# Kernel tuning notes

Hardware: AMD Instinct MI355X
Metric: run time of the kernel (lower is better)

## Reference

```python
import jax, jax.numpy as jnp
import numpy as np

N_NODES = 50000
IN_C = 128
OUT_C = 128
N_EDGES = 1600000
NEG_SLOPE = 0.2
EPS = 1e-16  # matches torch_geometric softmax denominator epsilon


def setup_inputs() -> dict:
    key = jax.random.key(0)
    k1, k2, k3, k4, k5 = jax.random.split(key, 5)
    glorot = 1.0 / np.sqrt(IN_C)
    x = jax.random.normal(k1, (N_NODES, IN_C), dtype=jnp.float32)
    W = jax.random.normal(k2, (IN_C, OUT_C), dtype=jnp.float32) * glorot
    a_src = jax.random.normal(k3, (OUT_C,), dtype=jnp.float32) * glorot
    a_dst = jax.random.normal(k4, (OUT_C,), dtype=jnp.float32) * glorot
    bias = jnp.zeros((OUT_C,), dtype=jnp.float32)
    edge_index = jax.random.randint(k5, (2, N_EDGES), 0, N_NODES, dtype=jnp.int32)
    return {"x": x, "W": W, "a_src": a_src, "a_dst": a_dst,
            "bias": bias, "edge_index": edge_index}


def reference(x, W, a_src, a_dst, bias, edge_index):
    N = x.shape[0]
    # add self loops (GATConv default add_self_loops=True)
    loops = jnp.arange(N, dtype=edge_index.dtype)
    src = jnp.concatenate([edge_index[0], loops])  # [E+N]
    dst = jnp.concatenate([edge_index[1], loops])

    h = x @ W                                      # [N, out]
    alpha_s = h @ a_src                            # [N]
    alpha_d = h @ a_dst                            # [N]

    e = alpha_s[src] + alpha_d[dst]                # [E+N]
    e = jnp.where(e > 0, e, NEG_SLOPE * e)         # leaky_relu

    # neighbor-wise (per destination node) stable softmax
    m = jax.ops.segment_max(e, dst, num_segments=N)
    ex = jnp.exp(e - m[dst])
    denom = jax.ops.segment_sum(ex, dst, num_segments=N)
    alpha = ex / (denom[dst] + EPS)

    # weighted aggregation of source features into destination nodes
    msgs = h[src] * alpha[:, None]                 # [E+N, out]
    out = jax.ops.segment_sum(msgs, dst, num_segments=N) + bias
    return jax.nn.relu(out)
```

## Files before the change

kernel.cpp:

```cpp
#include <hip/hip_runtime.h>
#include <hip/hip_fp16.h>

#define C 128
#define NEG_SLOPE 0.2f
#define SM_EPS 1e-16f
#define BKT_SHIFT 8
#define BKT_MASK 255
#define WP 136

typedef unsigned int uint32;
typedef __attribute__((ext_vector_type(8))) short bf16x8;
typedef __attribute__((ext_vector_type(4))) float f32x4;

static __device__ __forceinline__ unsigned short f2bf(float f) {
    uint32 u = __float_as_uint(f);
    uint32 r = 0x7FFFu + ((u >> 16) & 1u);
    return (unsigned short)((u + r) >> 16);
}
static __device__ __forceinline__ uint32 f2bf2(float lo, float hi) {
    return (uint32)f2bf(lo) | ((uint32)f2bf(hi) << 16);
}
static __device__ __forceinline__ uint32 f2h(float f) {
    __half h = __float2half(f);
    return (uint32)*reinterpret_cast<unsigned short*>(&h);
}
static __device__ __forceinline__ float h2f(uint32 b) {
    unsigned short s = (unsigned short)(b & 0xffffu);
    __half h = *reinterpret_cast<__half*>(&s);
    return __half2float(h);
}

__global__ __launch_bounds__(256) void cvtw_kernel(const float* __restrict__ W,
                                                   uint32* __restrict__ Wf) {
    int gid = blockIdx.x * 256 + threadIdx.x;
    int j2   = gid & 3;
    int lane = (gid >> 2) & 63;
    int tile = gid >> 8;
    int t = tile >> 2, kk = tile & 3;
    int n = t * 16 + (lane & 15);
    int k = kk * 32 + (lane >> 4) * 8 + j2 * 2;
    Wf[gid] = f2bf2(W[k * C + n], W[(k + 1) * C + n]);
}

__global__ __launch_bounds__(256) void gemm_hist_kernel(
    const float* __restrict__ x, const uint32* __restrict__ Wf,
    const float* __restrict__ a_src, const float* __restrict__ a_dst,
    unsigned short* __restrict__ hb, float* __restrict__ as_out,
    float* __restrict__ ad_out, int N,
    const int* __restrict__ dst, int* __restrict__ H,
    int E, int total, int chunkE)
{
    __shared__ __align__(16) unsigned short slice[4][16 * WP];
    __shared__ int lhist[256];

    const int tid  = threadIdx.x;
    const int lane = tid & 63;
    const int w    = tid >> 6;
    const int row0 = blockIdx.x * 64;
    const int m16  = lane & 15;
    const int q    = lane >> 4;

    lhist[tid] = 0;

    const int row = row0 + w * 16 + m16;
    const bool rv = (row < N);
    const float* xr_p = x + (size_t)(rv ? row : 0) * C + q * 8;

    float4 xr[8];
    #pragma unroll
    for (int kk = 0; kk < 4; ++kk) {
        xr[kk * 2]     = rv ? *(const float4*)(xr_p + kk * 32)     : make_float4(0, 0, 0, 0);
        xr[kk * 2 + 1] = rv ? *(const float4*)(xr_p + kk * 32 + 4) : make_float4(0, 0, 0, 0);
    }

    f32x4 acc[8];
    const f32x4 zz = {0.f, 0.f, 0.f, 0.f};
    #pragma unroll
    for (int t = 0; t < 8; ++t) acc[t] = zz;

    #pragma unroll
    for (int kk = 0; kk < 4; ++kk) {
        union { bf16x8 v; uint32 u[4]; } au;
        float4 p0 = xr[kk * 2], p1 = xr[kk * 2 + 1];
        au.u[0] = f2bf2(p0.x, p0.y); au.u[1] = f2bf2(p0.z, p0.w);
        au.u[2] = f2bf2(p1.x, p1.y); au.u[3] = f2bf2(p1.z, p1.w);
        #pragma unroll
        for (int t = 0; t < 8; ++t) {
            bf16x8 b = *(const bf16x8*)&Wf[((t * 4 + kk) * 64 + lane) * 4];
            acc[t] = __builtin_amdgcn_mfma_f32_16x16x32_bf16(au.v, b, acc[t], 0, 0, 0);
        }
    }

    float ps[4] = {0.f, 0.f, 0.f, 0.f}, pd[4] = {0.f, 0.f, 0.f, 0.f};
    #pragma unroll
    for (int t = 0; t < 8; ++t) {
        float av = a_src[t * 16 + m16];
        float dv = a_dst[t * 16 + m16];
        #pragma unroll
        for (int r = 0; r < 4; ++r) {
            ps[r] += acc[t][r] * av;
            pd[r] += acc[t][r] * dv;
        }
    }
    #pragma unroll
    for (int r = 0; r < 4; ++r) {
        #pragma unroll
        for (int off = 1; off < 16; off <<= 1) {
            ps[r] += __shfl_xor(ps[r], off, 64);
            pd[r] += __shfl_xor(pd[r], off, 64);
        }
    }
    if (m16 == 0) {
        #pragma unroll
        for (int r = 0; r < 4; ++r) {
            int rr = row0 + w * 16 + q * 4 + r;
            if (rr < N) { as_out[rr] = ps[r]; ad_out[rr] = pd[r]; }
        }
    }

    #pragma unroll
    for (int t = 0; t < 8; ++t)
        #pragma unroll
        for (int r = 0; r < 4; ++r)
            slice[w][(q * 4 + r) * WP + t * 16 + m16] = f2bf(acc[t][r]);
    __syncthreads();
    #pragma unroll
    for (int it = 0; it < 4; ++it) {
        int r = it * 4 + q;
        int rr = row0 + w * 16 + r;
        if (rr < N) {
            bf16x8 v = *(const bf16x8*)&slice[w][r * WP + m16 * 8];
            *(bf16x8*)&hb[(size_t)rr * C + m16 * 8] = v;
        }
    }

    const int c = blockIdx.x;
    const int start = c * chunkE;
    const int end = min(start + chunkE, total);
    for (int i = start + tid; i < end; i += 256) {
        int d = (i < E) ? dst[i] : (i - E);
        atomicAdd(&lhist[d >> BKT_SHIFT], 1);
    }
    __syncthreads();
    H[c * 256 + tid] = lhist[tid];
}

__global__ __launch_bounds__(1024) void scan_cols_kernel(
    int* __restrict__ H, int* __restrict__ colTot, int nchunk)
{
    __shared__ int wt[16];
    const int tid  = threadIdx.x;
    const int lane = tid & 63;
    const int w    = tid >> 6;
    const int col  = blockIdx.x;
    int v = (tid < nchunk) ? H[tid * 256 + col] : 0;
    int x = v;
    #pragma unroll
    for (int o = 1; o < 64; o <<= 1) {
        int t = __shfl_up(x, o, 64);
        if (lane >= o) x += t;
    }
    if (lane == 63) wt[w] = x;
    __syncthreads();
    int wbase = 0;
    #pragma unroll
    for (int w2 = 0; w2 < 16; ++w2) wbase += (w2 < w) ? wt[w2] : 0;
    int e = wbase + x - v;
    if (tid < nchunk) H[tid * 256 + col] = e;
    if (tid == nchunk - 1) colTot[col] = e + v;
}

__global__ __launch_bounds__(256) void scan_off_kernel(
    const int* __restrict__ colTot, int* __restrict__ bucket_off, int total)
{
    __shared__ int wt[4];
    const int tid = threadIdx.x;
    const int lane = tid & 63;
    const int w = tid >> 6;
    int v = colTot[tid];
    int x = v;
    #pragma unroll
    for (int o = 1; o < 64; o <<= 1) {
        int t = __shfl_up(x, o, 64);
        if (lane >= o) x += t;
    }
    if (lane == 63) wt[w] = x;
    __syncthreads();
    int wbase = 0;
    #pragma unroll
    for (int w2 = 0; w2 < 4; ++w2) wbase += (w2 < w) ? wt[w2] : 0;
    bucket_off[tid] = wbase + x - v;
    if (tid == 0) bucket_off[256] = total;
}

__global__ __launch_bounds__(256) void bin_kernel(
    const int* __restrict__ src, const int* __restrict__ dst,
    const int* __restrict__ bucket_off, const int* __restrict__ H,
    uint32* __restrict__ packed, int E, int total, int chunkE)
{
    __shared__ int lhist[256];
    __shared__ int base[256];
    const int tid = threadIdx.x;
    const int c = blockIdx.x;
    const int start = c * chunkE;
    const int end = min(start + chunkE, total);

    lhist[tid] = 0;
    __syncthreads();
    for (int i = start + tid; i < end; i += 256) {
        int d = (i < E) ? dst[i] : (i - E);
        atomicAdd(&lhist[d >> BKT_SHIFT], 1);
    }
    __syncthreads();
    base[tid] = bucket_off[tid] + H[c * 256 + tid];
    lhist[tid] = 0;
    __syncthreads();
    for (int i = start + tid; i < end; i += 256) {
        int s = (i < E) ? src[i] : (i - E);
        int d = (i < E) ? dst[i] : (i - E);
        int b = d >> BKT_SHIFT;
        int pos = base[b] + atomicAdd(&lhist[b], 1);
        packed[pos] = ((uint32)s << BKT_SHIFT) | (uint32)(d & BKT_MASK);
    }
}

__global__ __launch_bounds__(1024) void build_kernel(
    const uint32* __restrict__ packed, const int* __restrict__ bucket_off,
    const float* __restrict__ as, const float* __restrict__ ad,
    int* __restrict__ row_start, uint32* __restrict__ csr, int N, int NB, int total)
{
    __shared__ int cnt[256];
    __shared__ int cur[256];
    __shared__ float adl[256];
    __shared__ int wt[4];
    const int tid = threadIdx.x;
    const int b = blockIdx.x;

    if (tid < 256) {
        cnt[tid] = 0;
        int g = (b << BKT_SHIFT) + tid;
        adl[tid] = (g < N) ? ad[g] : 0.f;
    }
    __syncthreads();
    const int off = bucket_off[b];
    const int end = bucket_off[b + 1];
    if (b == 0 && tid == 0) row_start[N] = total;

    for (int j = off + tid; j < end; j += 1024)
        atomicAdd(&cnt[packed[j] & BKT_MASK], 1);
    __syncthreads();

    int v2 = 0, x2 = 0;
    if (tid < 256) {
        const int lane = tid & 63;
        v2 = cnt[tid]; x2 = v2;
        #pragma unroll
        for (int o = 1; o < 64; o <<= 1) {
            int t = __shfl_up(x2, o, 64);
            if (lane >= o) x2 += t;
        }
        if (lane == 63) wt[tid >> 6] = x2;
    }
    __syncthreads();
    if (tid < 256) {
        const int w = tid >> 6;
        int wbase = 0;
        #pragma unroll
        for (int w2 = 0; w2 < 4; ++w2) wbase += (w2 < w) ? wt[w2] : 0;
        int excl = wbase + x2 - v2;
        int g = (b << BKT_SHIFT) + tid;
        if (g < N) row_start[g] = off + excl;
        cur[tid] = excl;
    }
    __syncthreads();

    for (int j = off + tid; j < end; j += 1024) {
        uint32 p = packed[j];
        int l = (int)(p & BKT_MASK);
        int s = (int)(p >> BKT_SHIFT);
        float e = as[s] + adl[l];
        e = (e > 0.f) ? e : NEG_SLOPE * e;
        int pos = atomicAdd(&cur[l], 1);
        csr[off + pos] = ((uint32)s << 16) | f2h(e);
    }
}

static __device__ __forceinline__ void gather_node_fw(
    int d, const uint32* __restrict__ csr, const int* __restrict__ row_start,
    const unsigned short* __restrict__ hb, const float* __restrict__ bias,
    float* __restrict__ out, int lane)
{
    const int beg = row_start[d];
    const int deg = row_start[d + 1] - beg;
    const int c2 = lane << 1;
    float a0 = 0.f, a1 = 0.f;
    float m = -INFINITY;
    for (int t = lane; t < deg; t += 64) m = fmaxf(m, h2f(csr[beg + t]));
    #pragma unroll
    for (int off = 32; off > 0; off >>= 1) m = fmaxf(m, __shfl_xor(m, off, 64));
    float ssum = 0.f;
    for (int t = lane; t < deg; t += 64) ssum += __expf(h2f(csr[beg + t]) - m);
    #pragma unroll
    for (int off = 32; off > 0; off >>= 1) ssum += __shfl_xor(ssum, off, 64);
    float inv = 1.f / (ssum + SM_EPS);
    for (int t0 = 0; t0 < deg; t0 += 64) {
        int nc = min(64, deg - t0);
        uint32 ent = (lane < nc) ? csr[beg + t0 + lane] : 0xFC00u;
        float wl = (lane < nc) ? __expf(h2f(ent) - m) * inv : 0.f;
        uint32 bc = (ent & 0xffff0000u) | f2h(wl);
        for (int t = 0; t < nc; ++t) {
            uint32 b0 = (uint32)__shfl((int)bc, t, 64);
            uint32 u0 = *(const uint32*)&hb[(size_t)(b0 >> 16) * C + c2];
            float w0 = h2f(b0);
            a0 += __uint_as_float(u0 << 16) * w0;
            a1 += __uint_as_float(u0 & 0xffff0000u) * w0;
        }
    }
    float2 b2 = *(const float2*)&bias[c2];
    a0 = fmaxf(a0 + b2.x, 0.f);
    a1 = fmaxf(a1 + b2.y, 0.f);
    *(float2*)&out[(size_t)d * C + c2] = make_float2(a0, a1);
}

#define ACC4(r, wgt)                                           \
    {                                                          \
        a0 += __uint_as_float((r).x << 16)         * (wgt);    \
        a1 += __uint_as_float((r).x & 0xffff0000u) * (wgt);    \
        a2 += __uint_as_float((r).y << 16)         * (wgt);    \
        a3 += __uint_as_float((r).y & 0xffff0000u) * (wgt);    \
    }

__global__ __launch_bounds__(256) void gather_kernel(
    const uint32* __restrict__ csr, const int* __restrict__ row_start,
    const unsigned short* __restrict__ hb, const float* __restrict__ bias,
    float* __restrict__ out, int N)
{
    __shared__ __align__(16) uint2 lent[4][2][64];
    const int w    = threadIdx.x >> 6;
    const int lane = threadIdx.x & 63;
    const int half = lane >> 5;
    const int hl   = lane & 31;
    const int pair = blockIdx.x * 4 + w;
    const int d0 = pair * 2;
    if (d0 >= N) return;
    const int d = d0 + half;
    const bool valid = (d < N);

    int beg = 0, deg = 0;
    if (valid) { beg = row_start[d]; deg = row_start[d + 1] - beg; }

    int wdeg = deg;
    #pragma unroll
    for (int off = 32; off > 0; off >>= 1) wdeg = max(wdeg, __shfl_xor(wdeg, off, 64));

    if (wdeg > 64) {
        gather_node_fw(d0, csr, row_start, hb, bias, out, lane);
        if (d0 + 1 < N) gather_node_fw(d0 + 1, csr, row_start, hb, bias, out, lane);
        return;
    }

    uint32 ent0 = (hl < deg) ? csr[beg + hl] : 0xFC00u;
    uint32 ent1 = (32 + hl < deg) ? csr[beg + 32 + hl] : 0xFC00u;
    float e0 = h2f(ent0), e1 = h2f(ent1);
    float m = fmaxf(e0, e1);
    #pragma unroll
    for (int off = 16; off > 0; off >>= 1) m = fmaxf(m, __shfl_xor(m, off, 64));
    float p0 = (hl < deg) ? __expf(e0 - m) : 0.f;
    float p1 = (32 + hl < deg) ? __expf(e1 - m) : 0.f;
    float ssum = p0 + p1;
    #pragma unroll
    for (int off = 16; off > 0; off >>= 1) ssum += __shfl_xor(ssum, off, 64);
    const float inv = 1.f / (ssum + SM_EPS);

    lent[w][half][hl]      = make_uint2((ent0 & 0xffff0000u) >> 8, __float_as_uint(p0 * inv));
    lent[w][half][32 + hl] = make_uint2((ent1 & 0xffff0000u) >> 8, __float_as_uint(p1 * inv));
    __builtin_amdgcn_wave_barrier();

    const uint32 cb = (uint32)(hl << 3);
    const char* hbB = (const char*)hb;
    const uint2* lp = &lent[w][half][0];
    float a0 = 0.f, a1 = 0.f, a2 = 0.f, a3 = 0.f;

    int t = 0;
    for (; t + 8 <= deg; t += 8) {
        uint4 q0 = *(const uint4*)(lp + t);
        uint4 q1 = *(const uint4*)(lp + t + 2);
        uint4 q2 = *(const uint4*)(lp + t + 4);
        uint4 q3 = *(const uint4*)(lp + t + 6);
        uint2 r0 = *(const uint2*)(hbB + (q0.x + cb));
        uint2 r1 = *(const uint2*)(hbB + (q0.z + cb));
        uint2 r2 = *(const uint2*)(hbB + (q1.x + cb));
        uint2 r3 = *(const uint2*)(hbB + (q1.z + cb));
        uint2 r4 = *(const uint2*)(hbB + (q2.x + cb));
        uint2 r5 = *(const uint2*)(hbB + (q2.z + cb));
        uint2 r6 = *(const uint2*)(hbB + (q3.x + cb));
        uint2 r7 = *(const uint2*)(hbB + (q3.z + cb));
        float w0 = __uint_as_float(q0.y), w1 = __uint_as_float(q0.w);
        float w2 = __uint_as_float(q1.y), w3 = __uint_as_float(q1.w);
        float w4 = __uint_as_float(q2.y), w5 = __uint_as_float(q2.w);
        float w6 = __uint_as_float(q3.y), w7 = __uint_as_float(q3.w);
        ACC4(r0, w0) ACC4(r1, w1) ACC4(r2, w2) ACC4(r3, w3)
        ACC4(r4, w4) ACC4(r5, w5) ACC4(r6, w6) ACC4(r7, w7)
    }
    for (; t < deg; ++t) {
        uint2 q = lp[t];
        uint2 r = *(const uint2*)(hbB + (q.x + cb));
        float wt = __uint_as_float(q.y);
        ACC4(r, wt)
    }

    if (valid) {
        const int c4 = hl << 2;
        float4 bb = *(const float4*)&bias[c4];
        float4 o;
        o.x = fmaxf(a0 + bb.x, 0.f);
        o.y = fmaxf(a1 + bb.y, 0.f);
        o.z = fmaxf(a2 + bb.z, 0.f);
        o.w = fmaxf(a3 + bb.w, 0.f);
        *(float4*)&out[(size_t)d * C + c4] = o;
    }
}

extern "C" void kernel_launch(void* const* d_in, const int* in_sizes, int n_in,
                              void* d_out, int out_size, void* d_ws, size_t ws_size,
                              hipStream_t stream) {
    const float* x     = (const float*)d_in[0];
    const float* W     = (const float*)d_in[1];
    const float* a_src = (const float*)d_in[2];
    const float* a_dst = (const float*)d_in[3];
    const float* bias  = (const float*)d_in[4];
    const int*   edge  = (const int*)d_in[5];

    const int N = in_sizes[0] / C;
    const int E = in_sizes[5] / 2;
    const int total = E + N;
    const int* src = edge;
    const int* dst = edge + E;
    float* out = (float*)d_out;

    const int NB = (N + BKT_MASK) >> BKT_SHIFT;
    const int ntile = (N + 63) / 64;
    const int chunkE = (total + ntile - 1) / ntile;

    float* ws = (float*)d_ws;
    unsigned short* hb = (unsigned short*)ws;
    float* as = (float*)(hb + (size_t)N * C);
    float* ad = as + N;
    int* row_start = (int*)(ad + N);
    uint32* packed = (uint32*)(row_start + (N + 2));
    uint32* csr    = packed + total;
    uint32* Wf     = csr + total;
    int* colTot    = (int*)(Wf + 8192);
    int* bucket_off = colTot + 256;
    int* H          = bucket_off + 257;

    cvtw_kernel<<<32, 256, 0, stream>>>(W, Wf);
    gemm_hist_kernel<<<ntile, 256, 0, stream>>>(
        x, Wf, a_src, a_dst, hb, as, ad, N, dst, H, E, total, chunkE);
    scan_cols_kernel<<<256, 1024, 0, stream>>>(H, colTot, ntile);
    scan_off_kernel<<<1, 256, 0, stream>>>(colTot, bucket_off, total);
    bin_kernel<<<ntile, 256, 0, stream>>>(
        src, dst, bucket_off, H, packed, E, total, chunkE);
    build_kernel<<<NB, 1024, 0, stream>>>(packed, bucket_off, as, ad, row_start,
                                          csr, N, NB, total);
    gather_kernel<<<((N + 1) / 2 + 3) / 4, 256, 0, stream>>>(csr, row_start, hb, bias, out, N);
}
```

Baseline: 187.6 us.

## Split GEMM across bin/build kernels and compute attention logits via precomposed W·a

Attention scalars are now computed as x·(W·a) in fp32, with W·a precomputed alongside the weight conversion, instead of being taken from the bf16 GEMM accumulators. This lets the feature GEMM be split in half and co-scheduled with the binning and CSR build kernels in the same grid. The bucket width drops from 256 to 64 nodes, so there are more buckets with smaller histograms. The weight conversion and histogram kernels are merged, reducing launches, at the cost of an extra read of x for the logits and a larger histogram matrix.

Measured after the change: 230.3 us. 22.7% more time.

```diff
diff --git a/kernel.cpp b/kernel.cpp
--- a/kernel.cpp
+++ b/kernel.cpp
@@ -4,8 +4,9 @@
 #define C 128
 #define NEG_SLOPE 0.2f
 #define SM_EPS 1e-16f
-#define BKT_SHIFT 8
-#define BKT_MASK 255
+#define BKT_SHIFT 6
+#define BKT_MASK 63
+#define NBPAD 784
 #define WP 136
 
 typedef unsigned int uint32;
@@ -30,37 +31,18 @@
     return __half2float(h);
 }
 
-__global__ __launch_bounds__(256) void cvtw_kernel(const float* __restrict__ W,
-                                                   uint32* __restrict__ Wf) {
-    int gid = blockIdx.x * 256 + threadIdx.x;
-    int j2   = gid & 3;
-    int lane = (gid >> 2) & 63;
-    int tile = gid >> 8;
-    int t = tile >> 2, kk = tile & 3;
-    int n = t * 16 + (lane & 15);
-    int k = kk * 32 + (lane >> 4) * 8 + j2 * 2;
-    Wf[gid] = f2bf2(W[k * C + n], W[(k + 1) * C + n]);
-}
-
-__global__ __launch_bounds__(256) void gemm_hist_kernel(
+static __device__ __forceinline__ void gemm_tile_body(
     const float* __restrict__ x, const uint32* __restrict__ Wf,
-    const float* __restrict__ a_src, const float* __restrict__ a_dst,
-    unsigned short* __restrict__ hb, float* __restrict__ as_out,
-    float* __restrict__ ad_out, int N,
-    const int* __restrict__ dst, int* __restrict__ H,
-    int E, int total, int chunkE)
-{
-    __shared__ __align__(16) unsigned short slice[4][16 * WP];
-    __shared__ int lhist[256];
-
+    unsigned short* __restrict__ hb, int N, int tile, char* smem)
+{
+    typedef unsigned short SliceRow[16 * WP];
+    SliceRow* slice = (SliceRow*)smem;
     const int tid  = threadIdx.x;
     const int lane = tid & 63;
     const int w    = tid >> 6;
-    const int row0 = blockIdx.x * 64;
+    const int row0 = tile * 64;
     const int m16  = lane & 15;
     const int q    = lane >> 4;
-
-    lhist[tid] = 0;
 
     const int row = row0 + w * 16 + m16;
     const bool rv = (row < N);
@@ -91,33 +73,6 @@
         }
     }
 
-    float ps[4] = {0.f, 0.f, 0.f, 0.f}, pd[4] = {0.f, 0.f, 0.f, 0.f};
-    #pragma unroll
-    for (int t = 0; t < 8; ++t) {
-        float av = a_src[t * 16 + m16];
-        float dv = a_dst[t * 16 + m16];
-        #pragma unroll
-        for (int r = 0; r < 4; ++r) {
-            ps[r] += acc[t][r] * av;
-            pd[r] += acc[t][r] * dv;
-        }
-    }
-    #pragma unroll
-    for (int r = 0; r < 4; ++r) {
-        #pragma unroll
-        for (int off = 1; off < 16; off <<= 1) {
-            ps[r] += __shfl_xor(ps[r], off, 64);
-            pd[r] += __shfl_xor(pd[r], off, 64);
-        }
-    }
-    if (m16 == 0) {
-        #pragma unroll
-        for (int r = 0; r < 4; ++r) {
-            int rr = row0 + w * 16 + q * 4 + r;
-            if (rr < N) { as_out[rr] = ps[r]; ad_out[rr] = pd[r]; }
-        }
-    }
-
     #pragma unroll
     for (int t = 0; t < 8; ++t)
         #pragma unroll
@@ -133,8 +88,47 @@
             *(bf16x8*)&hb[(size_t)rr * C + m16 * 8] = v;
         }
     }
-
+}
+
+__global__ __launch_bounds__(256) void cvtw_hist_kernel(
+    const float* __restrict__ W, uint32* __restrict__ Wf,
+    const float* __restrict__ a_src, const float* __restrict__ a_dst,
+    float* __restrict__ wa_s, float* __restrict__ wa_d,
+    const int* __restrict__ dst, int* __restrict__ H,
+    int E, int total, int NB, int chunkE)
+{
+    __shared__ int lhist[NBPAD];
+    __shared__ float asd[256];
+    const int tid = threadIdx.x;
+    for (int i = tid; i < NBPAD; i += 256) lhist[i] = 0;
+    const int gid = blockIdx.x * 256 + tid;
+    if (gid < 8192) {
+        int j2   = gid & 3;
+        int lane = (gid >> 2) & 63;
+        int tile = gid >> 8;
+        int t = tile >> 2, kk = tile & 3;
+        int n = t * 16 + (lane & 15);
+        int k = kk * 32 + (lane >> 4) * 8 + j2 * 2;
+        Wf[gid] = f2bf2(W[k * C + n], W[(k + 1) * C + n]);
+    }
+    if (blockIdx.x == 32) {
+        asd[tid] = (tid < 128) ? a_src[tid] : a_dst[tid - 128];
+        __syncthreads();
+        const float* wrow = W + (size_t)(tid & 127) * C;
+        float acc = 0.f;
+        if (tid < 128) {
+            #pragma unroll 4
+            for (int j = 0; j < 128; ++j) acc += wrow[j] * asd[j];
+            wa_s[tid] = acc;
+        } else {
+            #pragma unroll 4
+            for (int j = 0; j < 128; ++j) acc += wrow[j] * asd[128 + j];
+            wa_d[tid - 128] = acc;
+        }
+    }
+    __syncthreads();
     const int c = blockIdx.x;
+    if (c >= NB) return;
     const int start = c * chunkE;
     const int end = min(start + chunkE, total);
     for (int i = start + tid; i < end; i += 256) {
@@ -142,18 +136,67 @@
         atomicAdd(&lhist[d >> BKT_SHIFT], 1);
     }
     __syncthreads();
-    H[c * 256 + tid] = lhist[tid];
-}
-
-__global__ __launch_bounds__(1024) void scan_cols_kernel(
-    int* __restrict__ H, int* __restrict__ colTot, int nchunk)
+    for (int b = tid; b < NBPAD; b += 256) H[c * NBPAD + b] = lhist[b];
+}
+
+__global__ __launch_bounds__(1024) void scan_alpha_kernel(
+    int* __restrict__ H, int* __restrict__ colTot,
+    const float* __restrict__ x, const float* __restrict__ wa_s,
+    const float* __restrict__ wa_d, float* __restrict__ as,
+    float* __restrict__ ad, int NB, int N)
+{
+    __shared__ int wt[16];
+    __shared__ float wls[128], wld[128];
+    const int tid  = threadIdx.x;
+    if (blockIdx.x < (unsigned)NB) {
+        const int lane = tid & 63;
+        const int w    = tid >> 6;
+        const int col  = blockIdx.x;
+        int v = (tid < NB) ? H[tid * NBPAD + col] : 0;
+        int x2 = v;
+        #pragma unroll
+        for (int o = 1; o < 64; o <<= 1) {
+            int t = __shfl_up(x2, o, 64);
+            if (lane >= o) x2 += t;
+        }
+        if (lane == 63) wt[w] = x2;
+        __syncthreads();
+        int wbase = 0;
+        #pragma unroll
+        for (int w2 = 0; w2 < 16; ++w2) wbase += (w2 < w) ? wt[w2] : 0;
+        int e = wbase + x2 - v;
+        if (tid < NB) H[tid * NBPAD + col] = e;
+        if (tid == NB - 1) colTot[col] = e + v;
+    } else {
+        if (tid < 128) wls[tid] = wa_s[tid];
+        else if (tid < 256) wld[tid - 128] = wa_d[tid - 128];
+        __syncthreads();
+        const int r = (blockIdx.x - NB) * 1024 + tid;
+        if (r < N) {
+            const float4* xr = (const float4*)(x + (size_t)r * C);
+            float s1 = 0.f, s2 = 0.f;
+            #pragma unroll 8
+            for (int j = 0; j < 32; ++j) {
+                float4 xv = xr[j];
+                float4 a = *(const float4*)&wls[j * 4];
+                float4 b = *(const float4*)&wld[j * 4];
+                s1 += xv.x * a.x + xv.y * a.y + xv.z * a.z + xv.w * a.w;
+                s2 += xv.x * b.x + xv.y * b.y + xv.z * b.z + xv.w * b.w;
+            }
+            as[r] = s1;
+            ad[r] = s2;
+        }
+    }
+}
+
+__global__ __launch_bounds__(1024) void scan_off_kernel(
+    const int* __restrict__ colTot, int* __restrict__ bucket_off, int NB)
 {
     __shared__ int wt[16];
     const int tid  = threadIdx.x;
     const int lane = tid & 63;
     const int w    = tid >> 6;
-    const int col  = blockIdx.x;
-    int v = (tid < nchunk) ? H[tid * 256 + col] : 0;
+    int v = (tid < NB) ? colTot[tid] : 0;
     int x = v;
     #pragma unroll
     for (int o = 1; o < 64; o <<= 1) {
@@ -165,123 +208,93 @@
     int wbase = 0;
     #pragma unroll
     for (int w2 = 0; w2 < 16; ++w2) wbase += (w2 < w) ? wt[w2] : 0;
-    int e = wbase + x - v;
-    if (tid < nchunk) H[tid * 256 + col] = e;
-    if (tid == nchunk - 1) colTot[col] = e + v;
-}
-
-__global__ __launch_bounds__(256) void scan_off_kernel(
-    const int* __restrict__ colTot, int* __restrict__ bucket_off, int total)
-{
-    __shared__ int wt[4];
-    const int tid = threadIdx.x;
-    const int lane = tid & 63;
-    const int w = tid >> 6;
-    int v = colTot[tid];
-    int x = v;
-    #pragma unroll
-    for (int o = 1; o < 64; o <<= 1) {
-        int t = __shfl_up(x, o, 64);
-        if (lane >= o) x += t;
-    }
-    if (lane == 63) wt[w] = x;
-    __syncthreads();
-    int wbase = 0;
-    #pragma unroll
-    for (int w2 = 0; w2 < 4; ++w2) wbase += (w2 < w) ? wt[w2] : 0;
-    bucket_off[tid] = wbase + x - v;
-    if (tid == 0) bucket_off[256] = total;
-}
-
-__global__ __launch_bounds__(256) void bin_kernel(
+    if (tid <= NB) bucket_off[tid] = wbase + x - v;
+}
+
+__global__ __launch_bounds__(256) void gemm_bin_kernel(
+    const float* __restrict__ x, const uint32* __restrict__ Wf,
+    unsigned short* __restrict__ hb, int N,
     const int* __restrict__ src, const int* __restrict__ dst,
     const int* __restrict__ bucket_off, const int* __restrict__ H,
-    uint32* __restrict__ packed, int E, int total, int chunkE)
-{
-    __shared__ int lhist[256];
-    __shared__ int base[256];
+    uint32* __restrict__ packed, int E, int total, int nG1, int NB, int chunkE)
+{
+    __shared__ __align__(16) char smem[17408];
     const int tid = threadIdx.x;
-    const int c = blockIdx.x;
-    const int start = c * chunkE;
-    const int end = min(start + chunkE, total);
-
-    lhist[tid] = 0;
-    __syncthreads();
-    for (int i = start + tid; i < end; i += 256) {
-        int d = (i < E) ? dst[i] : (i - E);
-        atomicAdd(&lhist[d >> BKT_SHIFT], 1);
-    }
-    __syncthreads();
-    base[tid] = bucket_off[tid] + H[c * 256 + tid];
-    lhist[tid] = 0;
-    __syncthreads();
-    for (int i = start + tid; i < end; i += 256) {
-        int s = (i < E) ? src[i] : (i - E);
-        int d = (i < E) ? dst[i] : (i - E);
-        int b = d >> BKT_SHIFT;
-        int pos = base[b] + atomicAdd(&lhist[b], 1);
-        packed[pos] = ((uint32)s << BKT_SHIFT) | (uint32)(d & BKT_MASK);
-    }
-}
-
-__global__ __launch_bounds__(1024) void build_kernel(
+    if (blockIdx.x < (unsigned)nG1) {
+        gemm_tile_body(x, Wf, hb, N, blockIdx.x, smem);
+    } else {
+        int* lhist = (int*)smem;
+        int* base  = lhist + NBPAD;
+        const int c = blockIdx.x - nG1;
+        for (int b = tid; b < NB; b += 256) {
+            lhist[b] = 0;
+            base[b] = bucket_off[b] + H[c * NBPAD + b];
+        }
+        __syncthreads();
+        const int start = c * chunkE;
+        const int end = min(start + chunkE, total);
+        for (int i = start + tid; i < end; i += 256) {
+            int s = (i < E) ? src[i] : (i - E);
+            int d = (i < E) ? dst[i] : (i - E);
+            int b = d >> BKT_SHIFT;
+            int pos = base[b] + atomicAdd(&lhist[b], 1);
+            packed[pos] = ((uint32)s << BKT_SHIFT) | (uint32)(d & BKT_MASK);
+        }
+    }
+}
+
+__global__ __launch_bounds__(256) void build_gemm_kernel(
+    const float* __restrict__ x, const uint32* __restrict__ Wf,
+    unsigned short* __restrict__ hb, int N,
     const uint32* __restrict__ packed, const int* __restrict__ bucket_off,
     const float* __restrict__ as, const float* __restrict__ ad,
-    int* __restrict__ row_start, uint32* __restrict__ csr, int N, int NB, int total)
-{
-    __shared__ int cnt[256];
-    __shared__ int cur[256];
-    __shared__ float adl[256];
-    __shared__ int wt[4];
+    int* __restrict__ row_start, uint32* __restrict__ csr,
+    int total, int nG1, int NB)
+{
+    __shared__ __align__(16) char smem[17408];
     const int tid = threadIdx.x;
-    const int b = blockIdx.x;
-
-    if (tid < 256) {
-        cnt[tid] = 0;
-        int g = (b << BKT_SHIFT) + tid;
-        adl[tid] = (g < N) ? ad[g] : 0.f;
-    }
-    __syncthreads();
-    const int off = bucket_off[b];
-    const int end = bucket_off[b + 1];
-    if (b == 0 && tid == 0) row_start[N] = total;
-
-    for (int j = off + tid; j < end; j += 1024)
-        atomicAdd(&cnt[packed[j] & BKT_MASK], 1);
-    __syncthreads();
-
-    int v2 = 0, x2 = 0;
-    if (tid < 256) {
-        const int lane = tid & 63;
-        v2 = cnt[tid]; x2 = v2;
-        #pragma unroll
-        for (int o = 1; o < 64; o <<= 1) {
-            int t = __shfl_up(x2, o, 64);
-            if (lane >= o) x2 += t;
-        }
-        if (lane == 63) wt[tid >> 6] = x2;
-    }
-    __syncthreads();
-    if (tid < 256) {
-        const int w = tid >> 6;
-        int wbase = 0;
-        #pragma unroll
-        for (int w2 = 0; w2 < 4; ++w2) wbase += (w2 < w) ? wt[w2] : 0;
-        int excl = wbase + x2 - v2;
-        int g = (b << BKT_SHIFT) + tid;
-        if (g < N) row_start[g] = off + excl;
-        cur[tid] = excl;
-    }
-    __syncthreads();
-
-    for (int j = off + tid; j < end; j += 1024) {
-        uint32 p = packed[j];
-        int l = (int)(p & BKT_MASK);
-        int s = (int)(p >> BKT_SHIFT);
-        float e = as[s] + adl[l];
-        e = (e > 0.f) ? e : NEG_SLOPE * e;
-        int pos = atomicAdd(&cur[l], 1);
-        csr[off + pos] = ((uint32)s << 16) | f2h(e);
+    if (blockIdx.x >= (unsigned)NB) {
+        gemm_tile_body(x, Wf, hb, N, nG1 + (blockIdx.x - NB), smem);
+    } else {
+        int* cnt   = (int*)smem;
+        int* cur   = cnt + 64;
+        float* adl = (float*)(cur + 64);
+        const int b = blockIdx.x;
+        const int off = bucket_off[b];
+        const int end = bucket_off[b + 1];
+        if (tid < 64) {
+            cnt[tid] = 0;
+            int g = (b << BKT_SHIFT) + tid;
+            adl[tid] = (g < N) ? ad[g] : 0.f;
+        }
+        if (b == 0 && tid == 0) row_start[N] = total;
+        __syncthreads();
+        for (int j = off + tid; j < end; j += 256)
+            atomicAdd(&cnt[packed[j] & BKT_MASK], 1);
+        __syncthreads();
+        if (tid < 64) {
+            int v = cnt[tid];
+            int x2 = v;
+            #pragma unroll
+            for (int o = 1; o < 64; o <<= 1) {
+                int t = __shfl_up(x2, o, 64);
+                if (tid >= o) x2 += t;
+            }
+            int excl = x2 - v;
+            int g = (b << BKT_SHIFT) + tid;
+            if (g < N) row_start[g] = off + excl;
+            cur[tid] = excl;
+        }
+        __syncthreads();
+        for (int j = off + tid; j < end; j += 256) {
+            uint32 p = packed[j];
+            int l = (int)(p & BKT_MASK);
+            int s = (int)(p >> BKT_SHIFT);
+            float e = as[s] + adl[l];
+            e = (e > 0.f) ? e : NEG_SLOPE * e;
+            int pos = atomicAdd(&cur[l], 1);
+            csr[off + pos] = ((uint32)s << 16) | f2h(e);
+        }
     }
 }
 
@@ -440,7 +453,8 @@
 
     const int NB = (N + BKT_MASK) >> BKT_SHIFT;
     const int ntile = (N + 63) / 64;
-    const int chunkE = (total + ntile - 1) / ntile;
+    const int chunkE = (total + NB - 1) / NB;
+    const int nG1 = (ntile + 1) / 2;
 
     float* ws = (float*)d_ws;
     unsigned short* hb = (unsigned short*)ws;
@@ -450,18 +464,23 @@
     uint32* packed = (uint32*)(row_start + (N + 2));
     uint32* csr    = packed + total;
     uint32* Wf     = csr + total;
-    int* colTot    = (int*)(Wf + 8192);
-    int* bucket_off = colTot + 256;
-    int* H          = bucket_off + 257;
-
-    cvtw_kernel<<<32, 256, 0, stream>>>(W, Wf);
-    gemm_hist_kernel<<<ntile, 256, 0, stream>>>(
-        x, Wf, a_src, a_dst, hb, as, ad, N, dst, H, E, total, chunkE);
-    scan_cols_kernel<<<256, 1024, 0, stream>>>(H, colTot, ntile);
-    scan_off_kernel<<<1, 256, 0, stream>>>(colTot, bucket_off, total);
-    bin_kernel<<<ntile, 256, 0, stream>>>(
-        src, dst, bucket_off, H, packed, E, total, chunkE);
-    build_kernel<<<NB, 1024, 0, stream>>>(packed, bucket_off, as, ad, row_start,
-                                          csr, N, NB, total);
+    float* wa_s    = (float*)(Wf + 8192);
+    float* wa_d    = wa_s + 128;
+    int* colTot    = (int*)(wa_d + 128);
+    int* bucket_off = colTot + NBPAD;
+    int* H          = bucket_off + NBPAD;
+
+    const int grid1 = (NB > 33) ? NB : 33;
+    const int nAlpha = (N + 1023) / 1024;
+
+    cvtw_hist_kernel<<<grid1, 256, 0, stream>>>(
+        W, Wf, a_src, a_dst, wa_s, wa_d, dst, H, E, total, NB, chunkE);
+    scan_alpha_kernel<<<NB + nAlpha, 1024, 0, stream>>>(
+        H, colTot, x, wa_s, wa_d, as, ad, NB, N);
+    scan_off_kernel<<<1, 1024, 0, stream>>>(colTot, bucket_off, NB);
+    gemm_bin_kernel<<<nG1 + NB, 256, 0, stream>>>(
+        x, Wf, hb, N, src, dst, bucket_off, H, packed, E, total, nG1, NB, chunkE);
+    build_gemm_kernel<<<NB + (ntile - nG1), 256, 0, stream>>>(
+        x, Wf, hb, N, packed, bucket_off, as, ad, row_start, csr, total, nG1, NB);
     gather_kernel<<<((N + 1) / 2 + 3) / 4, 256, 0, stream>>>(csr, row_start, hb, bias, out, N);
 }
```
